# Performance work log

Hardware: AMD Instinct MI355X
Metric: run time of the kernel (lower is better)

The kernel has to match this reference:

```python
import jax, jax.numpy as jnp
import numpy as np

NUM_HEADS = 12


def setup_inputs() -> dict:
    key = jax.random.key(0)
    ks = jax.random.split(key, 4)
    N, L, C = 32, 577, 768  # L = 24*24 patches + 1 cls token
    x = jax.random.normal(ks[0], (N, L, C), dtype=jnp.float32)
    w_qkv = jax.random.normal(ks[1], (3 * C, C), dtype=jnp.float32) * 0.02
    w_proj = jax.random.normal(ks[2], (C, C), dtype=jnp.float32) * 0.02
    b_proj = jnp.zeros((C,), dtype=jnp.float32)
    w_dwc = jax.random.normal(ks[3], (C, 1, 3, 3), dtype=jnp.float32) * 0.02
    b_dwc = jnp.zeros((C,), dtype=jnp.float32)
    return {"x": x, "w_qkv": w_qkv, "w_proj": w_proj, "b_proj": b_proj,
            "w_dwc": w_dwc, "b_dwc": b_dwc}


def reference(x, w_qkv, w_proj, b_proj, w_dwc, b_dwc):
    N, L, C = x.shape
    H = NUM_HEADS
    hd = C // H
    h = w = int(L ** 0.5)  # 24; h*w == L-1 (cls token excluded)

    # qkv transform: (N, L, 3C) -> (3, N, H, L, hd)
    qkv = (x @ w_qkv.T).reshape(N, L, 3, H, hd).transpose(2, 0, 3, 1, 4)
    q, k, v = qkv[0], qkv[1], qkv[2]

    # graph-candidate attention (default: scaled dot-product softmax)
    scale = hd ** -0.5
    scores = jnp.einsum('bhqd,bhkd->bhqk', q, k) * scale
    attn = jax.nn.softmax(scores, axis=-1)
    out = jnp.einsum('bhqk,bhkd->bhqd', attn, v)  # (N, H, L, hd)
    out = out.transpose(0, 2, 1, 3).reshape(N, L, C)

    # depthwise conv on v (patch tokens only), NCHW layout
    v_ = v[:, :, 1:, :].transpose(0, 2, 1, 3).reshape(N, h, w, C).transpose(0, 3, 1, 2)
    dwc = jax.lax.conv_general_dilated(
        v_, w_dwc, window_strides=(1, 1), padding=((1, 1), (1, 1)),
        dimension_numbers=('NCHW', 'OIHW', 'NCHW'), feature_group_count=C)
    dwc = dwc + b_dwc[None, :, None, None]
    dwc = dwc.transpose(0, 2, 3, 1).reshape(N, L - 1, C)

    out = out.at[:, 1:, :].add(dwc)
    out = out @ w_proj.T + b_proj
    return out
```

## Files before the change

kernel.cpp:

```cpp
#include <hip/hip_runtime.h>

typedef short bf16x8 __attribute__((ext_vector_type(8)));
typedef float f32x4 __attribute__((ext_vector_type(4)));
typedef unsigned short u16;
typedef __attribute__((address_space(3))) const u16* lds_cptr;

#define NB 32
#define LSEQ 577
#define CD 768
#define NH 12
#define HD 64
#define MROWS (NB * LSEQ)
#define LPAD 584

#define GLD16(g, l)                                                    \
  __builtin_amdgcn_global_load_lds(                                    \
      (const __attribute__((address_space(1))) void*)(g),              \
      (__attribute__((address_space(3))) void*)(l), 16, 0, 0)

#define DSR(dst, base, ofs)                                            \
  asm volatile("ds_read_b128 %0, %1 offset:" #ofs                      \
               : "=v"(dst) : "v"((lds_cptr)(base)))

__device__ __forceinline__ u16 f2bf(float f) {
  union { float f; unsigned u; } v; v.f = f;
  unsigned u = v.u + 0x7fffu + ((v.u >> 16) & 1u);
  return (u16)(u >> 16);
}
__device__ __forceinline__ float bf2f(u16 s) {
  union { unsigned u; float f; } v; v.u = ((unsigned)s) << 16;
  return v.f;
}

__global__ __launch_bounds__(256) void cvt_bf16(
    const float* __restrict__ src, u16* __restrict__ dst, int n4) {
  int i = blockIdx.x * 256 + threadIdx.x;
  if (i < n4) {
    float4 v = reinterpret_cast<const float4*>(src)[i];
    ushort4 o;
    o.x = f2bf(v.x); o.y = f2bf(v.y); o.z = f2bf(v.z); o.w = f2bf(v.w);
    reinterpret_cast<ushort4*>(dst)[i] = o;
  }
}

__global__ __launch_bounds__(512, 2) void qkv_gemm(
    const u16* __restrict__ xb, const u16* __restrict__ wqb,
    u16* __restrict__ qb, u16* __restrict__ kb, u16* __restrict__ vtb) {
  __shared__ __align__(16) u16 As[3][256 * 32];
  __shared__ __align__(16) u16 Bs[3][128 * 32];
  const int id = blockIdx.x;
  const int xcd = id & 7, pos = id >> 3;
  const int wg = (xcd < 2 ? xcd * 165 + pos : 330 + (xcd - 2) * 164 + pos);
  const int m0 = (wg / 18) * 256;
  const int n0 = (wg % 18) * 128;
  const int t = threadIdx.x;
  const int lane = t & 63, wid = t >> 6;
  const int wm = wid >> 1, wn = wid & 1;
  const int g = lane >> 4, cl = lane & 15;

  const int r16 = lane >> 2;
  const int scol = (lane & 3) * 8;
  const int ra0 = wid * 16 + r16;
  const int ra1 = 128 + wid * 16 + r16;
  int gm0 = m0 + ra0; gm0 = gm0 < MROWS ? gm0 : MROWS - 1;
  int gm1 = m0 + ra1; gm1 = gm1 < MROWS ? gm1 : MROWS - 1;
  const u16* ax0 = xb + (size_t)gm0 * CD + scol;
  const u16* ax1 = xb + (size_t)gm1 * CD + scol;
  const u16* bx0 = wqb + (size_t)(n0 + ra0) * CD + scol;

  const f32x4 fz = {0.f, 0.f, 0.f, 0.f};
  f32x4 acc[4][4];
#pragma unroll
  for (int i = 0; i < 4; ++i)
#pragma unroll
    for (int j = 0; j < 4; ++j) acc[i][j] = fz;

#define QSTAGE(b, kt)                                  \
  do {                                                 \
    int kc = (kt) * 32;                                \
    GLD16(ax0 + kc, &As[b][wid * 512]);                \
    GLD16(ax1 + kc, &As[b][(wid + 8) * 512]);          \
    GLD16(bx0 + kc, &Bs[b][wid * 512]);                \
  } while (0)

  QSTAGE(0, 0);
  QSTAGE(1, 1);
  for (int kt = 0; kt < 24; ++kt) {
    const int cb = kt % 3;
    if (kt < 23) asm volatile("s_waitcnt vmcnt(3)");
    else         asm volatile("s_waitcnt vmcnt(0)");
    __builtin_amdgcn_s_barrier();
    if (kt < 22) QSTAGE((kt + 2) % 3, kt + 2);
    const u16* pa = &As[cb][(wm * 64 + cl) * 32 + g * 8];
    const u16* pb = &Bs[cb][(wn * 64 + cl) * 32 + g * 8];
    bf16x8 af[4], bfv[4];
    DSR(af[0], pa, 0);    DSR(af[1], pa, 1024);
    DSR(af[2], pa, 2048); DSR(af[3], pa, 3072);
    DSR(bfv[0], pb, 0);    DSR(bfv[1], pb, 1024);
    DSR(bfv[2], pb, 2048); DSR(bfv[3], pb, 3072);
    asm volatile("s_waitcnt lgkmcnt(0)");
    __builtin_amdgcn_sched_barrier(0);
    __builtin_amdgcn_s_setprio(1);
#pragma unroll
    for (int mt = 0; mt < 4; ++mt)
#pragma unroll
      for (int nt = 0; nt < 4; ++nt)
        acc[mt][nt] = __builtin_amdgcn_mfma_f32_16x16x32_bf16(af[mt], bfv[nt], acc[mt][nt], 0, 0, 0);
    __builtin_amdgcn_s_setprio(0);
  }
#undef QSTAGE

  const int which = n0 / CD;
  const int rem0 = n0 % CD;
#pragma unroll
  for (int mt = 0; mt < 4; ++mt) {
#pragma unroll
    for (int nt = 0; nt < 4; ++nt) {
      int rem = rem0 + wn * 64 + nt * 16 + cl;
      int hh = rem >> 6, d = rem & 63;
#pragma unroll
      for (int r = 0; r < 4; ++r) {
        int m = m0 + wm * 64 + mt * 16 + g * 4 + r;
        if (m < MROWS) {
          int nb = m / LSEQ, l = m - nb * LSEQ;
          if (which == 0)
            qb[(((size_t)nb * NH + hh) * LSEQ + l) * HD + d] = f2bf(acc[mt][nt][r] * 0.125f);
          else if (which == 1)
            kb[(((size_t)nb * NH + hh) * LSEQ + l) * HD + d] = f2bf(acc[mt][nt][r]);
          else
            vtb[(((size_t)nb * NH + hh) * HD + d) * LPAD + l] = f2bf(acc[mt][nt][r]);
        }
      }
    }
  }
}

__global__ __launch_bounds__(512) void attn_fwd(
    const u16* __restrict__ q, const u16* __restrict__ k,
    const u16* __restrict__ vt, u16* __restrict__ y) {
  __shared__ __align__(16) u16 Ks[2][64 * 72];
  __shared__ __align__(16) u16 Vts[2][64 * 72];
  __shared__ __align__(16) u16 Ps[8][16 * 72];

  const int qtile = blockIdx.x;
  const int h = blockIdx.y;
  const int nb = blockIdx.z;
  const int tid = threadIdx.x;
  const int lane = tid & 63, wid = tid >> 6;
  const int g = lane >> 4, cl = lane & 15;

  const size_t hoff = ((size_t)nb * NH + h) * LSEQ * HD;
  const u16* qh = q + hoff;
  const u16* kh = k + hoff;
  const u16* vth = vt + ((size_t)nb * NH + h) * HD * LPAD;

  const int qbase = qtile * 128;
  const int qrow = qbase + wid * 16 + cl;
  const int qrc = qrow < LSEQ ? qrow : LSEQ - 1;
  bf16x8 qf0 = *reinterpret_cast<const bf16x8*>(qh + (size_t)qrc * HD + g * 8);
  bf16x8 qf1 = *reinterpret_cast<const bf16x8*>(qh + (size_t)qrc * HD + 32 + g * 8);

  const f32x4 fz = {0.f, 0.f, 0.f, 0.f};
  float mrow = -3.0e38f, lrow = 0.f;
  f32x4 oaccT[4];
#pragma unroll
  for (int dt = 0; dt < 4; ++dt) oaccT[dt] = fz;

  const int srow = tid >> 3, sc8 = (tid & 7) << 3;
  const u16* kptr = kh + (size_t)srow * HD + sc8;
  const u16* vptr = vth + (size_t)srow * LPAD + sc8;

  {
    uint4 kd = *reinterpret_cast<const uint4*>(kptr);
    uint4 vd = *reinterpret_cast<const uint4*>(vptr);
    *reinterpret_cast<uint4*>(&Ks[0][srow * 72 + sc8]) = kd;
    *reinterpret_cast<uint4*>(&Vts[0][srow * 72 + sc8]) = vd;
  }
  __syncthreads();

  const int NT = 10;
  for (int tt = 0; tt < NT; ++tt) {
    const int c = tt & 1;
    const int kv = tt * 64;
    uint4 kn = {0, 0, 0, 0}, vn = {0, 0, 0, 0};
    const bool pre = (tt + 1 < NT);
    if (pre) {
      int grow = kv + 64 + srow;
      if (grow < LSEQ) kn = *reinterpret_cast<const uint4*>(kptr + (size_t)(kv + 64) * HD);
      vn = *reinterpret_cast<const uint4*>(vptr + (kv + 64));
    }

    f32x4 sT[4];
    __builtin_amdgcn_s_setprio(1);
#pragma unroll
    for (int nt = 0; nt < 4; ++nt) {
      bf16x8 a0 = *reinterpret_cast<const bf16x8*>(&Ks[c][(nt * 16 + cl) * 72 + g * 8]);
      bf16x8 a1 = *reinterpret_cast<const bf16x8*>(&Ks[c][(nt * 16 + cl) * 72 + 32 + g * 8]);
      f32x4 s = fz;
      s = __builtin_amdgcn_mfma_f32_16x16x32_bf16(a0, qf0, s, 0, 0, 0);
      s = __builtin_amdgcn_mfma_f32_16x16x32_bf16(a1, qf1, s, 0, 0, 0);
      sT[nt] = s;
    }
    __builtin_amdgcn_s_setprio(0);

#pragma unroll
    for (int nt = 0; nt < 4; ++nt)
#pragma unroll
      for (int r = 0; r < 4; ++r)
        if (kv + nt * 16 + g * 4 + r >= LSEQ) sT[nt][r] = -3.0e38f;

    float pm = -3.0e38f;
#pragma unroll
    for (int nt = 0; nt < 4; ++nt)
#pragma unroll
      for (int r = 0; r < 4; ++r) pm = fmaxf(pm, sT[nt][r]);
    pm = fmaxf(pm, __shfl_xor(pm, 16));
    pm = fmaxf(pm, __shfl_xor(pm, 32));

    float nm = fmaxf(mrow, pm);
    float alpha = __expf(mrow - nm);
    mrow = nm;
    float ps = 0.f;
#pragma unroll
    for (int nt = 0; nt < 4; ++nt)
#pragma unroll
      for (int r = 0; r < 4; ++r) {
        float p = __expf(sT[nt][r] - nm);
        sT[nt][r] = p;
        ps += p;
      }
    ps += __shfl_xor(ps, 16);
    ps += __shfl_xor(ps, 32);
    lrow = lrow * alpha + ps;
#pragma unroll
    for (int dt = 0; dt < 4; ++dt) oaccT[dt] *= alpha;

#pragma unroll
    for (int nt = 0; nt < 4; ++nt) {
      ushort4 p4;
      p4.x = f2bf(sT[nt][0]); p4.y = f2bf(sT[nt][1]);
      p4.z = f2bf(sT[nt][2]); p4.w = f2bf(sT[nt][3]);
      *reinterpret_cast<ushort4*>(&Ps[wid][cl * 72 + nt * 16 + g * 4]) = p4;
    }

    __builtin_amdgcn_s_setprio(1);
#pragma unroll
    for (int kc = 0; kc < 2; ++kc) {
      bf16x8 pa = *reinterpret_cast<const bf16x8*>(&Ps[wid][cl * 72 + kc * 32 + g * 8]);
#pragma unroll
      for (int dt = 0; dt < 4; ++dt) {
        bf16x8 va = *reinterpret_cast<const bf16x8*>(&Vts[c][(dt * 16 + cl) * 72 + kc * 32 + g * 8]);
        oaccT[dt] = __builtin_amdgcn_mfma_f32_16x16x32_bf16(va, pa, oaccT[dt], 0, 0, 0);
      }
    }
    __builtin_amdgcn_s_setprio(0);

    if (pre) {
      *reinterpret_cast<uint4*>(&Ks[c ^ 1][srow * 72 + sc8]) = kn;
      *reinterpret_cast<uint4*>(&Vts[c ^ 1][srow * 72 + sc8]) = vn;
    }
    __syncthreads();
  }

  if (qrow < LSEQ) {
    float inv = 1.f / lrow;
#pragma unroll
    for (int dt = 0; dt < 4; ++dt) {
      ushort4 o4;
      o4.x = f2bf(oaccT[dt][0] * inv); o4.y = f2bf(oaccT[dt][1] * inv);
      o4.z = f2bf(oaccT[dt][2] * inv); o4.w = f2bf(oaccT[dt][3] * inv);
      *reinterpret_cast<ushort4*>(
          &y[((size_t)nb * LSEQ + qrow) * CD + h * HD + dt * 16 + g * 4]) = o4;
    }
  }
}

__global__ __launch_bounds__(256) void dwc_add(
    const u16* __restrict__ vt, const float* __restrict__ wd,
    const float* __restrict__ bd, u16* __restrict__ y) {
  __shared__ u16 V[32 * 588];
  const int d0 = blockIdx.x * 32;
  const int h = blockIdx.y;
  const int nb = blockIdx.z;
  const int t = threadIdx.x;
  const u16* vrow = vt + (((size_t)nb * NH + h) * HD + d0) * LPAD;

  for (int c = t; c < 32 * 73; c += 256) {
    int row = c / 73;
    int k0 = (c - row * 73) * 8;
    uint4 vv = *reinterpret_cast<const uint4*>(vrow + (size_t)row * LPAD + k0);
    const u16* vp = (const u16*)&vv;
    *reinterpret_cast<ushort4*>(&V[row * 588 + k0]) = *(const ushort4*)vp;
    *reinterpret_cast<ushort4*>(&V[row * 588 + k0 + 4]) = *(const ushort4*)(vp + 4);
  }
  __syncthreads();

  const int d = t & 31;
  const int c = h * HD + d0 + d;
  float w9[9];
#pragma unroll
  for (int j = 0; j < 9; ++j) w9[j] = wd[c * 9 + j];
  const float bias = bd[c];
  const u16* Vd = &V[d * 588];

  for (int it = 0; it < 72; ++it) {
    int li = (t >> 5) + it * 8;
    int py = li / 24, px = li - py * 24;
    float acc = bias;
#pragma unroll
    for (int ky = 0; ky < 3; ++ky) {
      int yy = py + ky - 1;
      if (yy < 0 || yy >= 24) continue;
      int base = 1 + yy * 24;
#pragma unroll
      for (int kx = 0; kx < 3; ++kx) {
        int xx = px + kx - 1;
        if (xx < 0 || xx >= 24) continue;
        acc += w9[ky * 3 + kx] * bf2f(Vd[base + xx]);
      }
    }
    size_t yi = ((size_t)nb * LSEQ + 1 + li) * CD + c;
    y[yi] = f2bf(bf2f(y[yi]) + acc);
  }
}

__global__ __launch_bounds__(256) void proj_gemm(
    const u16* __restrict__ yb, const u16* __restrict__ wpb,
    const float* __restrict__ bias, float* __restrict__ out) {
  __shared__ __align__(16) u16 As[2][128 * 32];
  __shared__ __align__(16) u16 Bs[2][128 * 32];
  const int id = blockIdx.x;
  const int xcd = id & 7, pos = id >> 3;
  const int wg = (xcd < 6 ? xcd * 109 + pos : 654 + (xcd - 6) * 108 + pos);
  const int m0 = (wg / 6) * 128;
  const int n0 = (wg % 6) * 128;
  const int t = threadIdx.x;
  const int lane = t & 63, wid = t >> 6;
  const int wm = wid >> 1, wn = wid & 1;
  const int g = lane >> 4, cl = lane & 15;

  const int srow = wid * 32 + (lane >> 2);
  const int scol = (lane & 3) * 8;
  int ga0 = m0 + srow;      ga0 = ga0 < MROWS ? ga0 : MROWS - 1;
  int ga1 = m0 + srow + 16; ga1 = ga1 < MROWS ? ga1 : MROWS - 1;
  const u16* asrc0 = yb + (size_t)ga0 * CD + scol;
  const u16* asrc1 = yb + (size_t)ga1 * CD + scol;
  const u16* bsrc0 = wpb + (size_t)(n0 + srow) * CD + scol;
  const u16* bsrc1 = wpb + (size_t)(n0 + srow + 16) * CD + scol;

  const f32x4 fz = {0.f, 0.f, 0.f, 0.f};
  f32x4 acc[4][4];
#pragma unroll
  for (int i = 0; i < 4; ++i)
#pragma unroll
    for (int j = 0; j < 4; ++j) acc[i][j] = fz;

#define PSTAGE(b, kt)                                   \
  do {                                                  \
    int kc = (kt) * 32;                                 \
    GLD16(asrc0 + kc, &As[b][wid * 1024]);              \
    GLD16(asrc1 + kc, &As[b][wid * 1024 + 512]);        \
    GLD16(bsrc0 + kc, &Bs[b][wid * 1024]);              \
    GLD16(bsrc1 + kc, &Bs[b][wid * 1024 + 512]);        \
  } while (0)

  PSTAGE(0, 0);
  __syncthreads();
  int cur = 0;
  for (int kt = 0; kt < 24; ++kt) {
    if (kt < 23) PSTAGE(cur ^ 1, kt + 1);
    bf16x8 af[4], bfv[4];
#pragma unroll
    for (int mt = 0; mt < 4; ++mt)
      af[mt] = *reinterpret_cast<const bf16x8*>(&As[cur][(wm * 64 + mt * 16 + cl) * 32 + g * 8]);
#pragma unroll
    for (int nt = 0; nt < 4; ++nt)
      bfv[nt] = *reinterpret_cast<const bf16x8*>(&Bs[cur][(wn * 64 + nt * 16 + cl) * 32 + g * 8]);
    __builtin_amdgcn_s_setprio(1);
#pragma unroll
    for (int mt = 0; mt < 4; ++mt)
#pragma unroll
      for (int nt = 0; nt < 4; ++nt)
        acc[mt][nt] = __builtin_amdgcn_mfma_f32_16x16x32_bf16(af[mt], bfv[nt], acc[mt][nt], 0, 0, 0);
    __builtin_amdgcn_s_setprio(0);
    __syncthreads();
    cur ^= 1;
  }
#undef PSTAGE

#pragma unroll
  for (int nt = 0; nt < 4; ++nt) {
    int n = n0 + wn * 64 + nt * 16 + cl;
    float bn = bias[n];
#pragma unroll
    for (int mt = 0; mt < 4; ++mt)
#pragma unroll
      for (int r = 0; r < 4; ++r) {
        int m = m0 + wm * 64 + mt * 16 + g * 4 + r;
        if (m < MROWS) out[(size_t)m * CD + n] = acc[mt][nt][r] + bn;
      }
  }
}

extern "C" void kernel_launch(void* const* d_in, const int* in_sizes, int n_in,
                              void* d_out, int out_size, void* d_ws, size_t ws_size,
                              hipStream_t stream) {
  const float* x = (const float*)d_in[0];
  const float* w_qkv = (const float*)d_in[1];
  const float* w_proj = (const float*)d_in[2];
  const float* b_proj = (const float*)d_in[3];
  const float* w_dwc = (const float*)d_in[4];
  const float* b_dwc = (const float*)d_in[5];
  float* out = (float*)d_out;

  const size_t SEG = (size_t)NB * NH * LSEQ * HD;
  const size_t SEGT = (size_t)NB * NH * HD * LPAD;
  const size_t YN = (size_t)MROWS * CD;
  u16* yb = (u16*)d_ws;
  u16* xb = yb;
  u16* qb = yb + YN;
  u16* kb = qb + SEG;
  u16* vtb = kb + SEG;
  u16* wqb = vtb + SEGT;
  u16* wpb = wqb + (size_t)3 * CD * CD;

  cvt_bf16<<<dim3((int)(YN / 4 / 256)), 256, 0, stream>>>(x, xb, (int)(YN / 4));
  cvt_bf16<<<dim3(3 * CD * CD / 4 / 256), 256, 0, stream>>>(w_qkv, wqb, 3 * CD * CD / 4);
  cvt_bf16<<<dim3(CD * CD / 4 / 256), 256, 0, stream>>>(w_proj, wpb, CD * CD / 4);
  qkv_gemm<<<dim3(1314), 512, 0, stream>>>(xb, wqb, qb, kb, vtb);
  attn_fwd<<<dim3(5, 12, 32), 512, 0, stream>>>(qb, kb, vtb, yb);
  dwc_add<<<dim3(2, 12, 32), 256, 0, stream>>>(vtb, w_dwc, b_dwc, yb);
  proj_gemm<<<dim3(870), 256, 0, stream>>>(yb, wpb, b_proj, out);
}
```

Before: 357.8 us.

## Use exp2 lazy-rescale softmax and triple-buffered 256x128 proj GEMM

Folds log2(e) into the Q scaling so the attention kernel can use exp2f. It skips the running-max rescale of the accumulators unless a new block max exceeds the current one by more than 8, a bound that keeps exp2 values in range. The projection GEMM is rebuilt with 512-thread blocks, 256x128 tiles and a three-stage LDS buffer. That buffer is driven by explicit vmcnt waits and inline ds_read_b128, which cuts the number of barriers and overlaps loads with MFMA work, at the cost of more LDS and fewer blocks.

After: 352.2 us. No clear change (-1.6%).

```diff
diff --git a/kernel.cpp b/kernel.cpp
--- a/kernel.cpp
+++ b/kernel.cpp
@@ -124,7 +124,7 @@
         if (m < MROWS) {
           int nb = m / LSEQ, l = m - nb * LSEQ;
           if (which == 0)
-            qb[(((size_t)nb * NH + hh) * LSEQ + l) * HD + d] = f2bf(acc[mt][nt][r] * 0.125f);
+            qb[(((size_t)nb * NH + hh) * LSEQ + l) * HD + d] = f2bf(acc[mt][nt][r] * 0.18033688f);
           else if (which == 1)
             kb[(((size_t)nb * NH + hh) * LSEQ + l) * HD + d] = f2bf(acc[mt][nt][r]);
           else
@@ -217,23 +217,26 @@
     pm = fmaxf(pm, __shfl_xor(pm, 16));
     pm = fmaxf(pm, __shfl_xor(pm, 32));
 
-    float nm = fmaxf(mrow, pm);
-    float alpha = __expf(mrow - nm);
-    mrow = nm;
+    if (!__all(pm <= mrow + 8.0f)) {
+      float nm = fmaxf(mrow, pm);
+      float alpha = exp2f(mrow - nm);
+      lrow *= alpha;
+#pragma unroll
+      for (int dt = 0; dt < 4; ++dt) oaccT[dt] *= alpha;
+      mrow = nm;
+    }
     float ps = 0.f;
 #pragma unroll
     for (int nt = 0; nt < 4; ++nt)
 #pragma unroll
       for (int r = 0; r < 4; ++r) {
-        float p = __expf(sT[nt][r] - nm);
+        float p = exp2f(sT[nt][r] - mrow);
         sT[nt][r] = p;
         ps += p;
       }
     ps += __shfl_xor(ps, 16);
     ps += __shfl_xor(ps, 32);
-    lrow = lrow * alpha + ps;
-#pragma unroll
-    for (int dt = 0; dt < 4; ++dt) oaccT[dt] *= alpha;
+    lrow += ps;
 
 #pragma unroll
     for (int nt = 0; nt < 4; ++nt) {
@@ -324,29 +327,30 @@
   }
 }
 
-__global__ __launch_bounds__(256) void proj_gemm(
+__global__ __launch_bounds__(512, 2) void proj_gemm(
     const u16* __restrict__ yb, const u16* __restrict__ wpb,
     const float* __restrict__ bias, float* __restrict__ out) {
-  __shared__ __align__(16) u16 As[2][128 * 32];
-  __shared__ __align__(16) u16 Bs[2][128 * 32];
+  __shared__ __align__(16) u16 As[3][256 * 32];
+  __shared__ __align__(16) u16 Bs[3][128 * 32];
   const int id = blockIdx.x;
   const int xcd = id & 7, pos = id >> 3;
-  const int wg = (xcd < 6 ? xcd * 109 + pos : 654 + (xcd - 6) * 108 + pos);
-  const int m0 = (wg / 6) * 128;
+  const int wg = (xcd < 6 ? xcd * 55 + pos : 330 + (xcd - 6) * 54 + pos);
+  const int m0 = (wg / 6) * 256;
   const int n0 = (wg % 6) * 128;
   const int t = threadIdx.x;
   const int lane = t & 63, wid = t >> 6;
   const int wm = wid >> 1, wn = wid & 1;
   const int g = lane >> 4, cl = lane & 15;
 
-  const int srow = wid * 32 + (lane >> 2);
+  const int r16 = lane >> 2;
   const int scol = (lane & 3) * 8;
-  int ga0 = m0 + srow;      ga0 = ga0 < MROWS ? ga0 : MROWS - 1;
-  int ga1 = m0 + srow + 16; ga1 = ga1 < MROWS ? ga1 : MROWS - 1;
-  const u16* asrc0 = yb + (size_t)ga0 * CD + scol;
-  const u16* asrc1 = yb + (size_t)ga1 * CD + scol;
-  const u16* bsrc0 = wpb + (size_t)(n0 + srow) * CD + scol;
-  const u16* bsrc1 = wpb + (size_t)(n0 + srow + 16) * CD + scol;
+  const int ra0 = wid * 16 + r16;
+  const int ra1 = 128 + wid * 16 + r16;
+  int gm0 = m0 + ra0; gm0 = gm0 < MROWS ? gm0 : MROWS - 1;
+  int gm1 = m0 + ra1; gm1 = gm1 < MROWS ? gm1 : MROWS - 1;
+  const u16* ax0 = yb + (size_t)gm0 * CD + scol;
+  const u16* ax1 = yb + (size_t)gm1 * CD + scol;
+  const u16* bx0 = wpb + (size_t)(n0 + ra0) * CD + scol;
 
   const f32x4 fz = {0.f, 0.f, 0.f, 0.f};
   f32x4 acc[4][4];
@@ -355,27 +359,31 @@
 #pragma unroll
     for (int j = 0; j < 4; ++j) acc[i][j] = fz;
 
-#define PSTAGE(b, kt)                                   \
-  do {                                                  \
-    int kc = (kt) * 32;                                 \
-    GLD16(asrc0 + kc, &As[b][wid * 1024]);              \
-    GLD16(asrc1 + kc, &As[b][wid * 1024 + 512]);        \
-    GLD16(bsrc0 + kc, &Bs[b][wid * 1024]);              \
-    GLD16(bsrc1 + kc, &Bs[b][wid * 1024 + 512]);        \
+#define PSTAGE(b, kt)                                  \
+  do {                                                 \
+    int kc = (kt) * 32;                                \
+    GLD16(ax0 + kc, &As[b][wid * 512]);                \
+    GLD16(ax1 + kc, &As[b][(wid + 8) * 512]);          \
+    GLD16(bx0 + kc, &Bs[b][wid * 512]);                \
   } while (0)
 
   PSTAGE(0, 0);
-  __syncthreads();
-  int cur = 0;
+  PSTAGE(1, 1);
   for (int kt = 0; kt < 24; ++kt) {
-    if (kt < 23) PSTAGE(cur ^ 1, kt + 1);
+    const int cb = kt % 3;
+    if (kt < 23) asm volatile("s_waitcnt vmcnt(3)");
+    else         asm volatile("s_waitcnt vmcnt(0)");
+    __builtin_amdgcn_s_barrier();
+    if (kt < 22) PSTAGE((kt + 2) % 3, kt + 2);
+    const u16* pa = &As[cb][(wm * 64 + cl) * 32 + g * 8];
+    const u16* pb = &Bs[cb][(wn * 64 + cl) * 32 + g * 8];
     bf16x8 af[4], bfv[4];
-#pragma unroll
-    for (int mt = 0; mt < 4; ++mt)
-      af[mt] = *reinterpret_cast<const bf16x8*>(&As[cur][(wm * 64 + mt * 16 + cl) * 32 + g * 8]);
-#pragma unroll
-    for (int nt = 0; nt < 4; ++nt)
-      bfv[nt] = *reinterpret_cast<const bf16x8*>(&Bs[cur][(wn * 64 + nt * 16 + cl) * 32 + g * 8]);
+    DSR(af[0], pa, 0);    DSR(af[1], pa, 1024);
+    DSR(af[2], pa, 2048); DSR(af[3], pa, 3072);
+    DSR(bfv[0], pb, 0);    DSR(bfv[1], pb, 1024);
+    DSR(bfv[2], pb, 2048); DSR(bfv[3], pb, 3072);
+    asm volatile("s_waitcnt lgkmcnt(0)");
+    __builtin_amdgcn_sched_barrier(0);
     __builtin_amdgcn_s_setprio(1);
 #pragma unroll
     for (int mt = 0; mt < 4; ++mt)
@@ -383,8 +391,6 @@
       for (int nt = 0; nt < 4; ++nt)
         acc[mt][nt] = __builtin_amdgcn_mfma_f32_16x16x32_bf16(af[mt], bfv[nt], acc[mt][nt], 0, 0, 0);
     __builtin_amdgcn_s_setprio(0);
-    __syncthreads();
-    cur ^= 1;
   }
 #undef PSTAGE
 
@@ -430,5 +436,5 @@
   qkv_gemm<<<dim3(1314), 512, 0, stream>>>(xb, wqb, qb, kb, vtb);
   attn_fwd<<<dim3(5, 12, 32), 512, 0, stream>>>(qb, kb, vtb, yb);
   dwc_add<<<dim3(2, 12, 32), 256, 0, stream>>>(vtb, w_dwc, b_dwc, yb);
-  proj_gemm<<<dim3(870), 256, 0, stream>>>(yb, wpb, b_proj, out);
-}
+  proj_gemm<<<dim3(438), 512, 0, stream>>>(yb, wpb, b_proj, out);
+}
```
